# Optimization experiments

Hardware: AMD Instinct MI355X
Metric: run time of the kernel (lower is better)

Reference implementation:

```python
import jax, jax.numpy as jnp
import numpy as np

D_IN = 1024
D_OUT = 1024
NUM_HEADS = 16
HEAD_DIM = D_OUT // NUM_HEADS
SEQ = 2048
BATCH = 4


def setup_inputs() -> dict:
    key = jax.random.key(0)
    ks = jax.random.split(key, 6)
    s_in = 1.0 / np.sqrt(D_IN)
    s_out = 1.0 / np.sqrt(D_OUT)
    return {
        "inputs": jax.random.normal(ks[0], (BATCH, SEQ, D_IN), dtype=jnp.float32),
        # nn.Linear stores weight as [out, in]; y = x @ W.T
        "W_q": jax.random.uniform(ks[1], (D_OUT, D_IN), jnp.float32, -s_in, s_in),
        "W_k": jax.random.uniform(ks[2], (D_OUT, D_IN), jnp.float32, -s_in, s_in),
        "W_v": jax.random.uniform(ks[3], (D_OUT, D_IN), jnp.float32, -s_in, s_in),
        "W_o": jax.random.uniform(ks[4], (D_OUT, D_OUT), jnp.float32, -s_out, s_out),
        "b_o": jax.random.uniform(ks[5], (D_OUT,), jnp.float32, -s_out, s_out),
    }


def reference(inputs, W_q, W_k, W_v, W_o, b_o):
    B, T, _ = inputs.shape
    # projections: [B, T, d_out] -> [B, H, T, hd]
    def split_heads(x):
        return x.reshape(B, T, NUM_HEADS, HEAD_DIM).transpose(0, 2, 1, 3)

    Q = split_heads(inputs @ W_q.T)
    K = split_heads(inputs @ W_k.T)
    V = split_heads(inputs @ W_v.T)

    # [B, H, T, T] causal attention scores
    scores = jnp.einsum("bhqd,bhkd->bhqk", Q, K)
    causal = jnp.tril(jnp.ones((T, T), dtype=bool))  # True = keep
    scores = jnp.where(causal, scores, -jnp.inf)
    weights = jax.nn.softmax(scores / np.sqrt(HEAD_DIM), axis=-1)
    # dropout p=0.0 (eval mode): identity

    ctx = jnp.einsum("bhqk,bhkd->bhqd", weights, V)
    ctx = ctx.transpose(0, 2, 1, 3).reshape(B, T, D_OUT)
    return ctx @ W_o.T + b_o
```

## Files before the change

kernel.cpp:

```cpp
#include <hip/hip_runtime.h>
#include <cstdint>
#include <cstddef>

#define D_MODEL 1024
#define SEQQ    2048
#define NBATCH  4
#define NHEAD   16
#define HDIM    64
#define MTOT    (NBATCH * SEQQ)

typedef __attribute__((ext_vector_type(8))) short short8;
typedef __attribute__((ext_vector_type(4))) float floatx4;
typedef unsigned short u16;

__device__ __forceinline__ u16 f2bf(float f) {
  union { float f; uint32_t u; } a; a.f = f;
  uint32_t u = a.u;
  u += 0x7fffu + ((u >> 16) & 1u);
  return (u16)(u >> 16);
}

__device__ __forceinline__ floatx4 mfma16(short8 a, short8 b, floatx4 c) {
  return __builtin_amdgcn_mfma_f32_16x16x32_bf16(a, b, c, 0, 0, 0);
}

__device__ __forceinline__ void load_lds16(const void* g, void* l) {
  __builtin_amdgcn_global_load_lds(
      (const __attribute__((address_space(1))) uint32_t*)g,
      (__attribute__((address_space(3))) uint32_t*)l, 16, 0, 0);
}

__global__ __launch_bounds__(256) void k_cast_all(
    const float* __restrict__ X, const float* __restrict__ w0,
    const float* __restrict__ w1, const float* __restrict__ w2,
    const float* __restrict__ w3,
    u16* __restrict__ xb, u16* __restrict__ y0, u16* __restrict__ y1,
    u16* __restrict__ y2, u16* __restrict__ y3) {
  const int bx = blockIdx.x;
  const float* src; u16* dst; int i;
  if (bx < 8192) {
    src = X; dst = xb; i = (bx * 256 + threadIdx.x) * 4;
  } else {
    const int w = (bx - 8192) >> 10;
    src = (w == 0) ? w0 : (w == 1) ? w1 : (w == 2) ? w2 : w3;
    dst = (w == 0) ? y0 : (w == 1) ? y1 : (w == 2) ? y2 : y3;
    i = (((bx - 8192) & 1023) * 256 + threadIdx.x) * 4;
  }
  float4 v = *(const float4*)(src + i);
  ushort4 o;
  o.x = f2bf(v.x); o.y = f2bf(v.y); o.z = f2bf(v.z); o.w = f2bf(v.w);
  *(ushort4*)(dst + i) = o;
}

__global__ __launch_bounds__(256) void k_gemm_bt(
    const u16* __restrict__ A,
    const u16* __restrict__ B0, const u16* __restrict__ B1, const u16* __restrict__ B2,
    void* __restrict__ C0, void* __restrict__ C1, u16* __restrict__ VtOut,
    const float* __restrict__ bias, int M, int N, int K, int f32out, float ascaleQ) {
  __shared__ __align__(16) u16 As[2][128 * 64];
  __shared__ __align__(16) u16 Bs[2][128 * 64];
  const int tid = threadIdx.x;
  const int lane = tid & 63, wave = tid >> 6;
  const int quad = lane >> 4, l15 = lane & 15;

  const int bx = blockIdx.x;
  const int swz = (bx & 7) * 64 + (bx >> 3);
  const int m0 = (swz >> 3) * 128, n0 = (swz & 7) * 128;

  const int wr = wave >> 1, wc = wave & 1;
  const u16* Bm = (blockIdx.z == 0) ? B0 : (blockIdx.z == 1 ? B1 : B2);
  void* Cm = (blockIdx.z == 0) ? C0 : C1;
  const float ascale = (blockIdx.z == 0) ? ascaleQ : 1.0f;

  floatx4 acc[4][4];
#pragma unroll
  for (int i = 0; i < 4; ++i)
#pragma unroll
    for (int j = 0; j < 4; ++j) acc[i][j] = (floatx4){0.f, 0.f, 0.f, 0.f};

  const int srow = tid >> 3;
  const int scolx = ((tid & 7) * 8) ^ ((srow & 7) * 8);
  const u16* Ag = A + (size_t)(m0 + srow) * K + scolx;
  const u16* Bg = Bm + (size_t)(n0 + srow) * K + scolx;

#define STAGE_AB(tt, buf)                                                            \
  {                                                                                  \
    const int kk_ = (tt) * 64;                                                       \
    _Pragma("unroll")                                                                \
    for (int p = 0; p < 4; ++p) {                                                    \
      load_lds16(Ag + (size_t)(p * 32) * K + kk_, &As[buf][p * 2048 + wave * 512]);  \
      load_lds16(Bg + (size_t)(p * 32) * K + kk_, &Bs[buf][p * 2048 + wave * 512]);  \
    }                                                                                \
  }

  const int nIt = K / 64;
  STAGE_AB(0, 0);

  for (int it = 0; it < nIt; ++it) {
    const int cur = it & 1;
    __syncthreads();
    if (it + 1 < nIt) STAGE_AB(it + 1, cur ^ 1);

    short8 af[2][4], bfg[2][4];
#pragma unroll
    for (int ks = 0; ks < 2; ++ks) {
      const int kkx = (ks * 32 + quad * 8) ^ ((l15 & 7) * 8);
#pragma unroll
      for (int i = 0; i < 4; ++i) {
        af[ks][i]  = *(const short8*)&As[cur][(wr * 64 + i * 16 + l15) * 64 + kkx];
        bfg[ks][i] = *(const short8*)&Bs[cur][(wc * 64 + i * 16 + l15) * 64 + kkx];
      }
    }
#pragma unroll
    for (int ks = 0; ks < 2; ++ks)
#pragma unroll
      for (int mi = 0; mi < 4; ++mi)
#pragma unroll
        for (int ni = 0; ni < 4; ++ni)
          acc[mi][ni] = mfma16(af[ks][mi], bfg[ks][ni], acc[mi][ni]);
  }
#undef STAGE_AB

  if (blockIdx.z == 2) {
#pragma unroll
    for (int mi = 0; mi < 4; ++mi) {
#pragma unroll
      for (int ni = 0; ni < 4; ++ni) {
        const int row = m0 + wr * 64 + mi * 16 + quad * 4;
        const int col = n0 + wc * 64 + ni * 16 + l15;
        const int b = row >> 11, t = row & 2047;
        const int h = col >> 6, d = col & 63;
        ushort4 pk;
        pk.x = f2bf(acc[mi][ni][0]); pk.y = f2bf(acc[mi][ni][1]);
        pk.z = f2bf(acc[mi][ni][2]); pk.w = f2bf(acc[mi][ni][3]);
        *(ushort4*)(VtOut + (((size_t)(b * 16 + h) * 64 + d) * SEQQ + t)) = pk;
      }
    }
    return;
  }
#pragma unroll
  for (int mi = 0; mi < 4; ++mi) {
#pragma unroll
    for (int ni = 0; ni < 4; ++ni) {
      const int row = m0 + wr * 64 + mi * 16 + quad * 4;
      const int col = n0 + wc * 64 + ni * 16 + l15;
      const float bv = bias ? bias[col] : 0.f;
#pragma unroll
      for (int r = 0; r < 4; ++r) {
        const float v = acc[mi][ni][r] * ascale + bv;
        if (f32out) ((float*)Cm)[(size_t)(row + r) * N + col] = v;
        else        ((u16*)Cm)[(size_t)(row + r) * N + col] = f2bf(v);
      }
    }
  }
}

__device__ __forceinline__ short8 mk8(uint32_t a, uint32_t b, uint32_t c, uint32_t d) {
  union { uint32_t u[4]; short8 s; } t;
  t.u[0] = a; t.u[1] = b; t.u[2] = c; t.u[3] = d;
  return t.s;
}

__device__ __forceinline__ void softmax_reg(
    const floatx4 (&st)[4], float& lp, uint32_t (&w)[4][2]) {
#pragma unroll
  for (int ni = 0; ni < 4; ++ni) {
    const float p0 = __builtin_amdgcn_exp2f(st[ni][0]);
    const float p1 = __builtin_amdgcn_exp2f(st[ni][1]);
    const float p2 = __builtin_amdgcn_exp2f(st[ni][2]);
    const float p3 = __builtin_amdgcn_exp2f(st[ni][3]);
    lp += (p0 + p1) + (p2 + p3);
    w[ni][0] = __builtin_amdgcn_perm(__float_as_uint(p1), __float_as_uint(p0), 0x07060302u);
    w[ni][1] = __builtin_amdgcn_perm(__float_as_uint(p3), __float_as_uint(p2), 0x07060302u);
  }
}

__device__ __forceinline__ short8 pf_prep(const uint32_t (&w)[4][2], int kc) {
  uint32_t y0 = w[2 * kc][0], z0 = w[2 * kc + 1][0];
  asm("v_permlane32_swap_b32 %0, %1" : "+v"(y0), "+v"(z0));
  asm("v_permlane16_swap_b32 %0, %1" : "+v"(y0), "+v"(z0));
  uint32_t y1 = w[2 * kc][1], z1 = w[2 * kc + 1][1];
  asm("v_permlane32_swap_b32 %0, %1" : "+v"(y1), "+v"(z1));
  asm("v_permlane16_swap_b32 %0, %1" : "+v"(y1), "+v"(z1));
  return mk8(y0, y1, z0, z1);
}

__global__ __launch_bounds__(512) void k_attn(
    const u16* __restrict__ Q, const u16* __restrict__ Kg,
    const u16* __restrict__ Vt, u16* __restrict__ O) {
  __shared__ __align__(16) u16 Ks[2][128 * 64];
  __shared__ __align__(16) u16 Vs[2][64 * 128];
  const int tid = threadIdx.x, lane = tid & 63, wave = tid >> 6;
  const int quad = lane >> 4, l15 = lane & 15;

  const int lin = blockIdx.x;
  const int c = lin & 255, k2 = lin >> 8;
  const int g = k2 ? (7 - (c & 7)) : (c & 7);
  const int bh = (c >> 3) | (k2 << 5);
  const int b = bh >> 4, h = bh & 15;

  const int wgrp = wave >> 2, wsub = wave & 3;
  const int a = 2 * g + wgrp;
  const int qwA = 64 * a + wsub * 16;
  const int qwB = SEQQ - 64 * (a + 1) + wsub * 16;
  const int nT = 16 - g;
  const int uB = 31 - a;

  const u16* kbase = Kg + (size_t)(b * SEQQ) * D_MODEL + h * HDIM;
  const u16* vbase = Vt + (size_t)bh * (HDIM * SEQQ);

  const int krow = tid >> 3;
  const int kcol = ((tid & 7) * 8) ^ ((krow & 7) * 8);
  const int vrow = tid >> 4;
  const int vslot = tid & 15;
  const int vcol = (vslot >> 3) * 64 + (((vslot & 7) ^ (vrow & 7)) * 8);

#define STAGE_KV(tt, buf)                                                           \
  {                                                                                 \
    const int kt_ = (tt) * 128;                                                     \
    load_lds16(kbase + (size_t)(kt_ + krow) * D_MODEL + kcol,                       \
               &Ks[buf][wave * 512]);                                               \
    load_lds16(kbase + (size_t)(kt_ + 64 + krow) * D_MODEL + kcol,                  \
               &Ks[buf][4096 + wave * 512]);                                        \
    load_lds16(vbase + (size_t)vrow * SEQQ + kt_ + vcol,                            \
               &Vs[buf][wave * 512]);                                               \
    load_lds16(vbase + (size_t)(32 + vrow) * SEQQ + kt_ + vcol,                     \
               &Vs[buf][4096 + wave * 512]);                                        \
  }

  STAGE_KV(0, 0);

  short8 qfA[2], qfB[2];
  {
    const u16* qa = Q + (size_t)(b * SEQQ + qwA + l15) * D_MODEL + h * HDIM;
    const u16* qb = Q + (size_t)(b * SEQQ + qwB + l15) * D_MODEL + h * HDIM;
#pragma unroll
    for (int ks = 0; ks < 2; ++ks) {
      qfA[ks] = *(const short8*)(qa + ks * 32 + quad * 8);
      qfB[ks] = *(const short8*)(qb + ks * 32 + quad * 8);
    }
  }

  floatx4 accA[4], accB[4];
  float lAp = 0.f, lBp = 0.f;
#pragma unroll
  for (int i = 0; i < 4; ++i) {
    accA[i] = (floatx4){0.f, 0.f, 0.f, 0.f};
    accB[i] = (floatx4){0.f, 0.f, 0.f, 0.f};
  }

  for (int t = 0; t < nT; ++t) {
    const int cur = t & 1;
    __syncthreads();
    if (t + 1 < nT) STAGE_KV(t + 1, cur ^ 1);

#pragma unroll
    for (int sub = 0; sub < 2; ++sub) {
      const int u = 2 * t + sub;
      const bool doA = (u <= a);
      const bool doB = (u <= uB);

      short8 kf[4][2];
#pragma unroll
      for (int ni = 0; ni < 4; ++ni)
#pragma unroll
        for (int ks = 0; ks < 2; ++ks)
          kf[ni][ks] = *(const short8*)&Ks[cur][(sub * 64 + ni * 16 + l15) * 64 +
                                               ((ks * 32 + quad * 8) ^ ((l15 & 7) * 8))];
      short8 vf[2][4];
#pragma unroll
      for (int kc = 0; kc < 2; ++kc)
#pragma unroll
        for (int di = 0; di < 4; ++di)
          vf[kc][di] = *(const short8*)&Vs[cur][(di * 16 + l15) * 128 + sub * 64 +
                                               ((kc * 32 + quad * 8) ^ ((l15 & 7) * 8))];

      uint32_t wA[4][2], wB[4][2];
      if (doA) {
        floatx4 st[4];
        __builtin_amdgcn_s_setprio(1);
#pragma unroll
        for (int ni = 0; ni < 4; ++ni) {
          floatx4 s = (floatx4){0.f, 0.f, 0.f, 0.f};
          s = mfma16(kf[ni][0], qfA[0], s);
          s = mfma16(kf[ni][1], qfA[1], s);
          st[ni] = s;
        }
        __builtin_amdgcn_s_setprio(0);
        if (u == a) {
          const int qg = qwA + l15;
#pragma unroll
          for (int ni = 0; ni < 4; ++ni) {
            const int kg = u * 64 + ni * 16 + quad * 4;
#pragma unroll
            for (int r = 0; r < 4; ++r)
              if (kg + r > qg) st[ni][r] = -1e30f;
          }
        }
        softmax_reg(st, lAp, wA);
      }
      if (doB) {
        floatx4 st[4];
        __builtin_amdgcn_s_setprio(1);
#pragma unroll
        for (int ni = 0; ni < 4; ++ni) {
          floatx4 s = (floatx4){0.f, 0.f, 0.f, 0.f};
          s = mfma16(kf[ni][0], qfB[0], s);
          s = mfma16(kf[ni][1], qfB[1], s);
          st[ni] = s;
        }
        __builtin_amdgcn_s_setprio(0);
        if (u == uB) {
          const int qg = qwB + l15;
#pragma unroll
          for (int ni = 0; ni < 4; ++ni) {
            const int kg = u * 64 + ni * 16 + quad * 4;
#pragma unroll
            for (int r = 0; r < 4; ++r)
              if (kg + r > qg) st[ni][r] = -1e30f;
          }
        }
        softmax_reg(st, lBp, wB);
      }
#pragma unroll
      for (int kc = 0; kc < 2; ++kc) {
        if (doA) {
          const short8 pfA = pf_prep(wA, kc);
          __builtin_amdgcn_s_setprio(1);
#pragma unroll
          for (int di = 0; di < 4; ++di)
            accA[di] = mfma16(pfA, vf[kc][di], accA[di]);
          __builtin_amdgcn_s_setprio(0);
        }
        if (doB) {
          const short8 pfB = pf_prep(wB, kc);
          __builtin_amdgcn_s_setprio(1);
#pragma unroll
          for (int di = 0; di < 4; ++di)
            accB[di] = mfma16(pfB, vf[kc][di], accB[di]);
          __builtin_amdgcn_s_setprio(0);
        }
      }
    }
  }

  lAp += __shfl_xor(lAp, 16); lAp += __shfl_xor(lAp, 32);
  lBp += __shfl_xor(lBp, 16); lBp += __shfl_xor(lBp, 32);

  {
    u16* orow = O + (size_t)(b * SEQQ + qwA + quad * 4) * D_MODEL + h * HDIM + l15;
#pragma unroll
    for (int r = 0; r < 4; ++r) {
      const float inv = 1.0f / __shfl(lAp, quad * 4 + r, 16);
#pragma unroll
      for (int di = 0; di < 4; ++di)
        orow[(size_t)r * D_MODEL + di * 16] = f2bf(accA[di][r] * inv);
    }
  }
  {
    u16* orow = O + (size_t)(b * SEQQ + qwB + quad * 4) * D_MODEL + h * HDIM + l15;
#pragma unroll
    for (int r = 0; r < 4; ++r) {
      const float inv = 1.0f / __shfl(lBp, quad * 4 + r, 16);
#pragma unroll
      for (int di = 0; di < 4; ++di)
        orow[(size_t)r * D_MODEL + di * 16] = f2bf(accB[di][r] * inv);
    }
  }
}

extern "C" void kernel_launch(void* const* d_in, const int* in_sizes, int n_in,
                              void* d_out, int out_size, void* d_ws, size_t ws_size,
                              hipStream_t stream) {
  const float* X  = (const float*)d_in[0];
  const float* Wq = (const float*)d_in[1];
  const float* Wk = (const float*)d_in[2];
  const float* Wv = (const float*)d_in[3];
  const float* Wo = (const float*)d_in[4];
  const float* bo = (const float*)d_in[5];
  float* out = (float*)d_out;

  u16* ws = (u16*)d_ws;
  const size_t NE = (size_t)MTOT * D_MODEL;
  u16* Xb  = ws;
  u16* Qb  = Xb + NE;
  u16* Kb  = Qb + NE;
  u16* Vt  = Kb + NE;
  u16* Cb  = Vt + NE;
  u16* Wqb = Cb + NE;
  u16* Wkb = Wqb + (size_t)D_MODEL * D_MODEL;
  u16* Wvb = Wkb + (size_t)D_MODEL * D_MODEL;
  u16* Wob = Wvb + (size_t)D_MODEL * D_MODEL;

  const float SCL2E = 0.18033688f;

  k_cast_all<<<12288, 256, 0, stream>>>(X, Wq, Wk, Wv, Wo, Xb, Wqb, Wkb, Wvb, Wob);

  k_gemm_bt<<<dim3(512, 1, 3), 256, 0, stream>>>(
      Xb, Wqb, Wkb, Wvb, Qb, Kb, Vt, nullptr, MTOT, D_MODEL, D_MODEL, 0, SCL2E);

  k_attn<<<512, 512, 0, stream>>>(Qb, Kb, Vt, Cb);

  k_gemm_bt<<<dim3(512, 1, 1), 256, 0, stream>>>(
      Cb, Wob, Wob, Wob, out, out, nullptr, bo, MTOT, D_MODEL, D_MODEL, 1, 1.0f);
}
```

Before: 248.3 us.

## Give each attention wave four query tiles and halve the attention block size

```diff
diff --git a/kernel.cpp b/kernel.cpp
--- a/kernel.cpp
+++ b/kernel.cpp
@@ -76,7 +76,7 @@
 #pragma unroll
   for (int i = 0; i < 4; ++i)
 #pragma unroll
-    for (int j = 0; j < 4; ++j) acc[i][j] = (floatx4){0.f, 0.f, 0.f, 0.f};
+    for (int jj = 0; jj < 4; ++jj) acc[i][jj] = (floatx4){0.f, 0.f, 0.f, 0.f};
 
   const int srow = tid >> 3;
   const int scolx = ((tid & 7) * 8) ^ ((srow & 7) * 8);
@@ -185,7 +185,7 @@
   return mk8(y0, y1, z0, z1);
 }
 
-__global__ __launch_bounds__(512) void k_attn(
+__global__ __launch_bounds__(256, 2) void k_attn(
     const u16* __restrict__ Q, const u16* __restrict__ Kg,
     const u16* __restrict__ Vt, u16* __restrict__ O) {
   __shared__ __align__(16) u16 Ks[2][128 * 64];
@@ -195,59 +195,58 @@
 
   const int lin = blockIdx.x;
   const int c = lin & 255, k2 = lin >> 8;
-  const int g = k2 ? (7 - (c & 7)) : (c & 7);
+  const int j = k2 ? (7 - (c & 7)) : (c & 7);
   const int bh = (c >> 3) | (k2 << 5);
   const int b = bh >> 4, h = bh & 15;
 
-  const int wgrp = wave >> 2, wsub = wave & 3;
-  const int a = 2 * g + wgrp;
-  const int qwA = 64 * a + wsub * 16;
-  const int qwB = SEQQ - 64 * (a + 1) + wsub * 16;
-  const int nT = 16 - g;
-  const int uB = 31 - a;
+  const int s = wave;
+  const int p1 = j, p2 = j + 8;
+  int lim[4], qw[4];
+  lim[0] = p1;      qw[0] = 64 * p1 + 16 * s;
+  lim[1] = 31 - p1; qw[1] = SEQQ - 64 * (p1 + 1) + 16 * s;
+  lim[2] = p2;      qw[2] = 64 * p2 + 16 * s;
+  lim[3] = 31 - p2; qw[3] = SEQQ - 64 * (p2 + 1) + 16 * s;
+  const int nSub = 32 - j;
+  const int nT = (nSub + 1) >> 1;
 
   const u16* kbase = Kg + (size_t)(b * SEQQ) * D_MODEL + h * HDIM;
   const u16* vbase = Vt + (size_t)bh * (HDIM * SEQQ);
 
   const int krow = tid >> 3;
   const int kcol = ((tid & 7) * 8) ^ ((krow & 7) * 8);
-  const int vrow = tid >> 4;
-  const int vslot = tid & 15;
+  const int vrow = tid >> 4, vslot = tid & 15;
   const int vcol = (vslot >> 3) * 64 + (((vslot & 7) ^ (vrow & 7)) * 8);
 
 #define STAGE_KV(tt, buf)                                                           \
   {                                                                                 \
     const int kt_ = (tt) * 128;                                                     \
-    load_lds16(kbase + (size_t)(kt_ + krow) * D_MODEL + kcol,                       \
-               &Ks[buf][wave * 512]);                                               \
-    load_lds16(kbase + (size_t)(kt_ + 64 + krow) * D_MODEL + kcol,                  \
-               &Ks[buf][4096 + wave * 512]);                                        \
-    load_lds16(vbase + (size_t)vrow * SEQQ + kt_ + vcol,                            \
-               &Vs[buf][wave * 512]);                                               \
-    load_lds16(vbase + (size_t)(32 + vrow) * SEQQ + kt_ + vcol,                     \
-               &Vs[buf][4096 + wave * 512]);                                        \
+    _Pragma("unroll")                                                               \
+    for (int c4 = 0; c4 < 4; ++c4)                                                  \
+      load_lds16(kbase + (size_t)(kt_ + c4 * 32 + krow) * D_MODEL + kcol,           \
+                 &Ks[buf][c4 * 2048 + wave * 512]);                                 \
+    _Pragma("unroll")                                                               \
+    for (int c4 = 0; c4 < 4; ++c4)                                                  \
+      load_lds16(vbase + (size_t)(c4 * 16 + vrow) * SEQQ + kt_ + vcol,              \
+                 &Vs[buf][c4 * 2048 + wave * 512]);                                 \
   }
 
   STAGE_KV(0, 0);
 
-  short8 qfA[2], qfB[2];
-  {
-    const u16* qa = Q + (size_t)(b * SEQQ + qwA + l15) * D_MODEL + h * HDIM;
-    const u16* qb = Q + (size_t)(b * SEQQ + qwB + l15) * D_MODEL + h * HDIM;
-#pragma unroll
-    for (int ks = 0; ks < 2; ++ks) {
-      qfA[ks] = *(const short8*)(qa + ks * 32 + quad * 8);
-      qfB[ks] = *(const short8*)(qb + ks * 32 + quad * 8);
-    }
-  }
-
-  floatx4 accA[4], accB[4];
-  float lAp = 0.f, lBp = 0.f;
-#pragma unroll
-  for (int i = 0; i < 4; ++i) {
-    accA[i] = (floatx4){0.f, 0.f, 0.f, 0.f};
-    accB[i] = (floatx4){0.f, 0.f, 0.f, 0.f};
-  }
+  short8 qf[4][2];
+#pragma unroll
+  for (int t4 = 0; t4 < 4; ++t4) {
+    const u16* qp = Q + (size_t)(b * SEQQ + qw[t4] + l15) * D_MODEL + h * HDIM;
+#pragma unroll
+    for (int ks = 0; ks < 2; ++ks)
+      qf[t4][ks] = *(const short8*)(qp + ks * 32 + quad * 8);
+  }
+
+  floatx4 acc[4][4];
+  float lp[4] = {0.f, 0.f, 0.f, 0.f};
+#pragma unroll
+  for (int t4 = 0; t4 < 4; ++t4)
+#pragma unroll
+    for (int i = 0; i < 4; ++i) acc[t4][i] = (floatx4){0.f, 0.f, 0.f, 0.f};
 
   for (int t = 0; t < nT; ++t) {
     const int cur = t & 1;
@@ -257,8 +256,6 @@
 #pragma unroll
     for (int sub = 0; sub < 2; ++sub) {
       const int u = 2 * t + sub;
-      const bool doA = (u <= a);
-      const bool doB = (u <= uB);
 
       short8 kf[4][2];
 #pragma unroll
@@ -267,6 +264,37 @@
         for (int ks = 0; ks < 2; ++ks)
           kf[ni][ks] = *(const short8*)&Ks[cur][(sub * 64 + ni * 16 + l15) * 64 +
                                                ((ks * 32 + quad * 8) ^ ((l15 & 7) * 8))];
+
+      uint32_t w[4][4][2];
+      bool act[4];
+#pragma unroll
+      for (int t4 = 0; t4 < 4; ++t4) {
+        act[t4] = (u <= lim[t4]);
+        if (act[t4]) {
+          floatx4 st[4];
+          __builtin_amdgcn_s_setprio(1);
+#pragma unroll
+          for (int ni = 0; ni < 4; ++ni) {
+            floatx4 sv = (floatx4){0.f, 0.f, 0.f, 0.f};
+            sv = mfma16(kf[ni][0], qf[t4][0], sv);
+            sv = mfma16(kf[ni][1], qf[t4][1], sv);
+            st[ni] = sv;
+          }
+          __builtin_amdgcn_s_setprio(0);
+          if (u == lim[t4]) {
+            const int qg = qw[t4] + l15;
+#pragma unroll
+            for (int ni = 0; ni < 4; ++ni) {
+              const int kg = u * 64 + ni * 16 + quad * 4;
+#pragma unroll
+              for (int r = 0; r < 4; ++r)
+                if (kg + r > qg) st[ni][r] = -1e30f;
+            }
+          }
+          softmax_reg(st, lp[t4], w[t4]);
+        }
+      }
+
       short8 vf[2][4];
 #pragma unroll
       for (int kc = 0; kc < 2; ++kc)
@@ -275,96 +303,34 @@
           vf[kc][di] = *(const short8*)&Vs[cur][(di * 16 + l15) * 128 + sub * 64 +
                                                ((kc * 32 + quad * 8) ^ ((l15 & 7) * 8))];
 
-      uint32_t wA[4][2], wB[4][2];
-      if (doA) {
-        floatx4 st[4];
-        __builtin_amdgcn_s_setprio(1);
-#pragma unroll
-        for (int ni = 0; ni < 4; ++ni) {
-          floatx4 s = (floatx4){0.f, 0.f, 0.f, 0.f};
-          s = mfma16(kf[ni][0], qfA[0], s);
-          s = mfma16(kf[ni][1], qfA[1], s);
-          st[ni] = s;
-        }
-        __builtin_amdgcn_s_setprio(0);
-        if (u == a) {
-          const int qg = qwA + l15;
-#pragma unroll
-          for (int ni = 0; ni < 4; ++ni) {
-            const int kg = u * 64 + ni * 16 + quad * 4;
-#pragma unroll
-            for (int r = 0; r < 4; ++r)
-              if (kg + r > qg) st[ni][r] = -1e30f;
+#pragma unroll
+      for (int kc = 0; kc < 2; ++kc) {
+#pragma unroll
+        for (int t4 = 0; t4 < 4; ++t4) {
+          if (act[t4]) {
+            const short8 pf = pf_prep(w[t4], kc);
+            __builtin_amdgcn_s_setprio(1);
+#pragma unroll
+            for (int di = 0; di < 4; ++di)
+              acc[t4][di] = mfma16(pf, vf[kc][di], acc[t4][di]);
+            __builtin_amdgcn_s_setprio(0);
           }
         }
-        softmax_reg(st, lAp, wA);
-      }
-      if (doB) {
-        floatx4 st[4];
-        __builtin_amdgcn_s_setprio(1);
-#pragma unroll
-        for (int ni = 0; ni < 4; ++ni) {
-          floatx4 s = (floatx4){0.f, 0.f, 0.f, 0.f};
-          s = mfma16(kf[ni][0], qfB[0], s);
-          s = mfma16(kf[ni][1], qfB[1], s);
-          st[ni] = s;
-        }
-        __builtin_amdgcn_s_setprio(0);
-        if (u == uB) {
-          const int qg = qwB + l15;
-#pragma unroll
-          for (int ni = 0; ni < 4; ++ni) {
-            const int kg = u * 64 + ni * 16 + quad * 4;
-#pragma unroll
-            for (int r = 0; r < 4; ++r)
-              if (kg + r > qg) st[ni][r] = -1e30f;
-          }
-        }
-        softmax_reg(st, lBp, wB);
-      }
-#pragma unroll
-      for (int kc = 0; kc < 2; ++kc) {
-        if (doA) {
-          const short8 pfA = pf_prep(wA, kc);
-          __builtin_amdgcn_s_setprio(1);
-#pragma unroll
-          for (int di = 0; di < 4; ++di)
-            accA[di] = mfma16(pfA, vf[kc][di], accA[di]);
-          __builtin_amdgcn_s_setprio(0);
-        }
-        if (doB) {
-          const short8 pfB = pf_prep(wB, kc);
-          __builtin_amdgcn_s_setprio(1);
-#pragma unroll
-          for (int di = 0; di < 4; ++di)
-            accB[di] = mfma16(pfB, vf[kc][di], accB[di]);
-          __builtin_amdgcn_s_setprio(0);
-        }
-      }
-    }
-  }
-
-  lAp += __shfl_xor(lAp, 16); lAp += __shfl_xor(lAp, 32);
-  lBp += __shfl_xor(lBp, 16); lBp += __shfl_xor(lBp, 32);
-
-  {
-    u16* orow = O + (size_t)(b * SEQQ + qwA + quad * 4) * D_MODEL + h * HDIM + l15;
+      }
+    }
+  }
+
+#pragma unroll
+  for (int t4 = 0; t4 < 4; ++t4) {
+    float l = lp[t4];
+    l += __shfl_xor(l, 16); l += __shfl_xor(l, 32);
+    u16* orow = O + (size_t)(b * SEQQ + qw[t4] + quad * 4) * D_MODEL + h * HDIM + l15;
 #pragma unroll
     for (int r = 0; r < 4; ++r) {
-      const float inv = 1.0f / __shfl(lAp, quad * 4 + r, 16);
+      const float inv = 1.0f / __shfl(l, quad * 4 + r, 16);
 #pragma unroll
       for (int di = 0; di < 4; ++di)
-        orow[(size_t)r * D_MODEL + di * 16] = f2bf(accA[di][r] * inv);
-    }
-  }
-  {
-    u16* orow = O + (size_t)(b * SEQQ + qwB + quad * 4) * D_MODEL + h * HDIM + l15;
-#pragma unroll
-    for (int r = 0; r < 4; ++r) {
-      const float inv = 1.0f / __shfl(lBp, quad * 4 + r, 16);
-#pragma unroll
-      for (int di = 0; di < 4; ++di)
-        orow[(size_t)r * D_MODEL + di * 16] = f2bf(accB[di][r] * inv);
+        orow[(size_t)r * D_MODEL + di * 16] = f2bf(acc[t4][di][r] * inv);
     }
   }
 }
@@ -399,7 +365,7 @@
   k_gemm_bt<<<dim3(512, 1, 3), 256, 0, stream>>>(
       Xb, Wqb, Wkb, Wvb, Qb, Kb, Vt, nullptr, MTOT, D_MODEL, D_MODEL, 0, SCL2E);
 
-  k_attn<<<512, 512, 0, stream>>>(Qb, Kb, Vt, Cb);
+  k_attn<<<512, 256, 0, stream>>>(Qb, Kb, Vt, Cb);
 
   k_gemm_bt<<<dim3(512, 1, 1), 256, 0, stream>>>(
       Cb, Wob, Wob, Wob, out, out, nullptr, bo, MTOT, D_MODEL, D_MODEL, 1, 1.0f);
```

Measured after the change: 243.8 us, median of 2. About the same (-1.8%).
